# Optimization experiments

Hardware: AMD Instinct MI355X
Metric: run time of the kernel (lower is better)

The kernel has to match this reference:

```python
import jax, jax.numpy as jnp
import numpy as np


def setup_inputs() -> dict:
    key0 = jax.random.key(0)
    kq, kk, kv = jax.random.split(key0, 3)
    B, S, E = 4, 2048, 1024
    query = jax.random.normal(kq, (B, S, E), dtype=jnp.float32)
    key = jax.random.normal(kk, (B, S, E), dtype=jnp.float32)
    value = jax.random.normal(kv, (B, S, E), dtype=jnp.float32)
    attn_mask = jnp.zeros((B, S, S), dtype=jnp.float32)
    return {"query": query, "key": key, "value": value, "attn_mask": attn_mask}


def reference(query, key, value, attn_mask):
    # qk = Q K^T / sqrt(E) + mask; softmax over last dim; dropout is
    # identity in eval mode (reference baseline); out = attn @ V.
    E = query.shape[-1]
    scale = 1.0 / jnp.sqrt(jnp.asarray(E, dtype=query.dtype))
    qk = jnp.einsum("bqe,bke->bqk", query, key) * scale + attn_mask
    attn = jax.nn.softmax(qk, axis=-1)
    out = jnp.einsum("bqk,bke->bqe", attn, value)
    return out
```

## Files before the change

### kernel.cpp

```cpp
#include <hip/hip_runtime.h>
#include <stdint.h>
#include <math.h>

typedef unsigned short u16;
typedef short bf16x8 __attribute__((ext_vector_type(8)));
typedef unsigned short u16x8 __attribute__((ext_vector_type(8)));
typedef unsigned short u16x4 __attribute__((ext_vector_type(4)));
typedef float f32x4 __attribute__((ext_vector_type(4)));

#define LOG2E 1.4426950408889634f

__device__ __forceinline__ float bf2f(u16 u) {
  union { unsigned int i; float f; } v; v.i = ((unsigned int)u) << 16; return v.f;
}
__device__ __forceinline__ u16 f2bf(float f) {
  union { float ff; unsigned int i; } v; v.ff = f;
  unsigned int x = v.i;
  return (u16)((x + 0x7FFFu + ((x >> 16) & 1u)) >> 16);
}

__global__ __launch_bounds__(256)
void cvt_f32_bf16(const float* __restrict__ src, u16* __restrict__ dst, long n)
{
  long i = ((long)blockIdx.x * 256 + threadIdx.x) * 8;
  if (i + 8 > n) return;
  f32x4 a = *(const f32x4*)&src[i];
  f32x4 b = *(const f32x4*)&src[i + 4];
  u16x8 o;
#pragma unroll
  for (int j = 0; j < 4; j++) { o[j] = f2bf(a[j]); o[4 + j] = f2bf(b[j]); }
  *(u16x8*)&dst[i] = o;
}

__global__ __launch_bounds__(256)
void transcvt_v(const float* __restrict__ V, u16* __restrict__ VT, int S, int E)
{
  __shared__ u16 t[64][72];
  const int b = blockIdx.z;
  const float* Vb = V + (long)b * S * E;
  u16* VTb = VT + (long)b * S * E;
  const int k0 = blockIdx.x * 64, n0 = blockIdx.y * 64;
  const int tid = threadIdx.x;
#pragma unroll
  for (int p = 0; p < 2; p++) {
    int kk = p * 32 + (tid >> 3);
    int nn = (tid & 7) * 8;
    f32x4 a = *(const f32x4*)&Vb[(long)(k0 + kk) * E + n0 + nn];
    f32x4 c = *(const f32x4*)&Vb[(long)(k0 + kk) * E + n0 + nn + 4];
#pragma unroll
    for (int j = 0; j < 4; j++) { t[nn + j][kk] = f2bf(a[j]); t[nn + 4 + j][kk] = f2bf(c[j]); }
  }
  __syncthreads();
#pragma unroll
  for (int p = 0; p < 2; p++) {
    int nn = p * 32 + (tid >> 3);
    int kk = (tid & 7) * 8;
    u16x8 u;
#pragma unroll
    for (int j = 0; j < 8; j++) u[j] = t[nn][kk + j];
    *(u16x8*)&VTb[(long)(n0 + nn) * S + k0 + kk] = u;
  }
}

template<int ASRC, int BSRC, int BMODE, int HASMASK, int COUT>
__global__ __launch_bounds__(256, 2)
void gemm_bt(const void* __restrict__ Ap, int lda, long aRowOff,
             const void* __restrict__ Bp, int ldb, long bBatchStride,
             void* __restrict__ Cp, int ldc, long cRowOff,
             const float* __restrict__ maskf,
             int K, float scale, long g0, int S)
{
  const int tid  = threadIdx.x;
  const int lane = tid & 63;
  const int wave = tid >> 6;
  const long gTile = g0 + (long)blockIdx.y * 128;
  const int  b     = (int)(gTile / S);
  const int  nTile = blockIdx.x * 128;

  __shared__ u16 As[128][40];
  __shared__ u16 Bs[128][40];

  const int qm = (wave >> 1) * 64;
  const int qn = (wave & 1) * 64;

  f32x4 acc[4][4];
#pragma unroll
  for (int i = 0; i < 4; i++)
#pragma unroll
    for (int j = 0; j < 4; j++) acc[i][j] = (f32x4){0.f, 0.f, 0.f, 0.f};

  const u16*   Ab = (const u16*)Ap   + (gTile - aRowOff) * (long)lda;
  const float* Af = (const float*)Ap + (gTile - aRowOff) * (long)lda;
  const u16*   Bb = (const u16*)Bp   + (long)b * bBatchStride;
  const float* Bf = (const float*)Bp + (long)b * bBatchStride;

  const int lm = lane & 15;
  const int lk = (lane >> 4) * 8;

  for (int k0 = 0; k0 < K; k0 += 32) {
    if (ASRC == 0) {
      int srow = tid >> 2, scol = (tid & 3) * 8;
#pragma unroll
      for (int p = 0; p < 2; p++) {
        int r = p * 64 + srow;
        *(u16x8*)&As[r][scol] = *(const u16x8*)&Ab[(long)r * lda + k0 + scol];
      }
    } else {
      int srow = tid >> 3, scol = (tid & 7) * 4;
#pragma unroll
      for (int p = 0; p < 4; p++) {
        int r = p * 32 + srow;
        f32x4 a = *(const f32x4*)&Af[(long)r * lda + k0 + scol];
        u16x4 o;
#pragma unroll
        for (int j = 0; j < 4; j++) o[j] = f2bf(a[j]);
        *(u16x4*)&As[r][scol] = o;
      }
    }
    if (BMODE == 0) {
      if (BSRC == 0) {
        int srow = tid >> 2, scol = (tid & 3) * 8;
#pragma unroll
        for (int p = 0; p < 2; p++) {
          int r = p * 64 + srow;
          *(u16x8*)&Bs[r][scol] = *(const u16x8*)&Bb[(long)(nTile + r) * ldb + k0 + scol];
        }
      } else {
        int srow = tid >> 3, scol = (tid & 7) * 4;
#pragma unroll
        for (int p = 0; p < 4; p++) {
          int r = p * 32 + srow;
          f32x4 a = *(const f32x4*)&Bf[(long)(nTile + r) * ldb + k0 + scol];
          u16x4 o;
#pragma unroll
          for (int j = 0; j < 4; j++) o[j] = f2bf(a[j]);
          *(u16x4*)&Bs[r][scol] = o;
        }
      }
    }
    __syncthreads();

    bf16x8 af[4], bfr[4];
#pragma unroll
    for (int rt = 0; rt < 4; rt++)
      af[rt] = *(const bf16x8*)&As[qm + rt * 16 + lm][lk];
    if (BMODE == 0) {
#pragma unroll
      for (int ct = 0; ct < 4; ct++)
        bfr[ct] = *(const bf16x8*)&Bs[qn + ct * 16 + lm][lk];
    } else {
#pragma unroll
      for (int ct = 0; ct < 4; ct++) {
        const float* vp = Bf + (long)(k0 + lk) * ldb + nTile + qn + ct * 16 + lm;
#pragma unroll
        for (int j = 0; j < 8; j++) bfr[ct][j] = (short)f2bf(vp[(long)j * ldb]);
      }
    }
#pragma unroll
    for (int rt = 0; rt < 4; rt++)
#pragma unroll
      for (int ct = 0; ct < 4; ct++)
        acc[rt][ct] = __builtin_amdgcn_mfma_f32_16x16x32_bf16(af[rt], bfr[ct], acc[rt][ct], 0, 0, 0);
    __syncthreads();
  }

  const int lr = (lane >> 4) * 4;
#pragma unroll
  for (int rt = 0; rt < 4; rt++) {
#pragma unroll
    for (int ct = 0; ct < 4; ct++) {
      long gr = gTile + qm + rt * 16 + lr;
      int  cc = nTile + qn + ct * 16 + lm;
#pragma unroll
      for (int i = 0; i < 4; i++) {
        float v = acc[rt][ct][i] * scale;
        if (HASMASK) v += maskf[(gr + i) * (long)ldc + cc];
        if (COUT == 0)
          ((u16*)Cp)[(gr + i - cRowOff) * (long)ldc + cc] = f2bf(v);
        else
          ((float*)Cp)[(gr + i - cRowOff) * (long)ldc + cc] = v;
      }
    }
  }
}

__global__ __launch_bounds__(256)
void softmax_rows(u16* __restrict__ Sbuf, int ncols)
{
  const long row = blockIdx.x;
  u16* rp = Sbuf + row * (long)ncols;
  const int tid = threadIdx.x;

  u16x8 u = *(const u16x8*)&rp[tid * 8];
  float x[8];
  float m = -3.0e38f;
#pragma unroll
  for (int i = 0; i < 8; i++) { x[i] = bf2f(u[i]); m = fmaxf(m, x[i]); }
#pragma unroll
  for (int off = 32; off; off >>= 1) m = fmaxf(m, __shfl_xor(m, off, 64));
  __shared__ float redm[4];
  if ((tid & 63) == 0) redm[tid >> 6] = m;
  __syncthreads();
  m = fmaxf(fmaxf(redm[0], redm[1]), fmaxf(redm[2], redm[3]));

  float e[8];
  float s = 0.f;
#pragma unroll
  for (int i = 0; i < 8; i++) { e[i] = exp2f((x[i] - m) * LOG2E); s += e[i]; }
#pragma unroll
  for (int off = 32; off; off >>= 1) s += __shfl_xor(s, off, 64);
  __shared__ float reds[4];
  if ((tid & 63) == 0) reds[tid >> 6] = s;
  __syncthreads();
  s = reds[0] + reds[1] + reds[2] + reds[3];

  float inv = 1.0f / s;
  u16x8 o;
#pragma unroll
  for (int i = 0; i < 8; i++) o[i] = f2bf(e[i] * inv);
  *(u16x8*)&rp[tid * 8] = o;
}

extern "C" void kernel_launch(void* const* d_in, const int* in_sizes, int n_in,
                              void* d_out, int out_size, void* d_ws, size_t ws_size,
                              hipStream_t stream)
{
  const float* Q    = (const float*)d_in[0];
  const float* Km   = (const float*)d_in[1];
  const float* V    = (const float*)d_in[2];
  const float* mask = (const float*)d_in[3];
  float* out = (float*)d_out;

  const long qsz = in_sizes[0];
  const long msz = in_sizes[3];
  const long E = 1024;
  const long S = (msz / qsz) * E;
  const long B = qsz / (S * E);
  const long G = B * S;
  const float scale = 1.0f / sqrtf((float)E);

  const size_t convBytes = (size_t)(3 * qsz) * 2;
  const size_t rowBytes  = (size_t)S * 2;
  char* w = (char*)d_ws;
  size_t avail = ws_size;
  const bool haveConv = (ws_size >= convBytes + 128 * rowBytes);

  u16 *Qb = nullptr, *Kb = nullptr, *VTb = nullptr;
  if (haveConv) {
    Qb  = (u16*)w;              w += (size_t)qsz * 2;
    Kb  = (u16*)w;              w += (size_t)qsz * 2;
    VTb = (u16*)w;              w += (size_t)qsz * 2;
    avail -= convBytes;
  }
  long Rmax = (long)((avail / rowBytes) / 128) * 128;
  if (Rmax > G) Rmax = G;
  if (Rmax < 128) Rmax = 128;
  u16* Sbuf = (u16*)w;

  if (haveConv) {
    cvt_f32_bf16<<<dim3((unsigned)(qsz / 2048)), 256, 0, stream>>>(Q, Qb, qsz);
    cvt_f32_bf16<<<dim3((unsigned)(qsz / 2048)), 256, 0, stream>>>(Km, Kb, qsz);
    transcvt_v<<<dim3(S / 64, E / 64, B), 256, 0, stream>>>(V, VTb, (int)S, (int)E);
  }

  for (long g0 = 0; g0 < G; g0 += Rmax) {
    const long R = (G - g0 < Rmax) ? (G - g0) : Rmax;
    if (haveConv) {
      gemm_bt<0, 0, 0, 1, 0><<<dim3(S / 128, R / 128), 256, 0, stream>>>(
          Qb, (int)E, 0L, Kb, (int)E, S * E,
          Sbuf, (int)S, g0, mask, (int)E, scale, g0, (int)S);
    } else {
      gemm_bt<1, 1, 0, 1, 0><<<dim3(S / 128, R / 128), 256, 0, stream>>>(
          Q, (int)E, 0L, Km, (int)E, S * E,
          Sbuf, (int)S, g0, mask, (int)E, scale, g0, (int)S);
    }
    softmax_rows<<<dim3(R), 256, 0, stream>>>(Sbuf, (int)S);
    if (haveConv) {
      gemm_bt<0, 0, 0, 0, 1><<<dim3(E / 128, R / 128), 256, 0, stream>>>(
          Sbuf, (int)S, g0, VTb, (int)S, E * S,
          out, (int)E, 0L, nullptr, (int)S, 1.0f, g0, (int)S);
    } else {
      gemm_bt<0, 1, 1, 0, 1><<<dim3(E / 128, R / 128), 256, 0, stream>>>(
          Sbuf, (int)S, g0, V, (int)E, S * E,
          out, (int)E, 0L, nullptr, (int)S, 1.0f, g0, (int)S);
    }
  }
}
```

Measured before the change: 302.4 us.

## Double-buffer GEMM LDS tiles and fuse Q/K bf16 conversion into QK GEMM

```diff
diff --git a/kernel.cpp b/kernel.cpp
--- a/kernel.cpp
+++ b/kernel.cpp
@@ -5,7 +5,6 @@
 typedef unsigned short u16;
 typedef short bf16x8 __attribute__((ext_vector_type(8)));
 typedef unsigned short u16x8 __attribute__((ext_vector_type(8)));
-typedef unsigned short u16x4 __attribute__((ext_vector_type(4)));
 typedef float f32x4 __attribute__((ext_vector_type(4)));
 
 #define LOG2E 1.4426950408889634f
@@ -17,19 +16,6 @@
   union { float ff; unsigned int i; } v; v.ff = f;
   unsigned int x = v.i;
   return (u16)((x + 0x7FFFu + ((x >> 16) & 1u)) >> 16);
-}
-
-__global__ __launch_bounds__(256)
-void cvt_f32_bf16(const float* __restrict__ src, u16* __restrict__ dst, long n)
-{
-  long i = ((long)blockIdx.x * 256 + threadIdx.x) * 8;
-  if (i + 8 > n) return;
-  f32x4 a = *(const f32x4*)&src[i];
-  f32x4 b = *(const f32x4*)&src[i + 4];
-  u16x8 o;
-#pragma unroll
-  for (int j = 0; j < 4; j++) { o[j] = f2bf(a[j]); o[4 + j] = f2bf(b[j]); }
-  *(u16x8*)&dst[i] = o;
 }
 
 __global__ __launch_bounds__(256)
@@ -62,10 +48,10 @@
   }
 }
 
-template<int ASRC, int BSRC, int BMODE, int HASMASK, int COUT>
+template<int ASRC_F32, int BSRC_F32, int HASMASK, int COUT>
 __global__ __launch_bounds__(256, 2)
-void gemm_bt(const void* __restrict__ Ap, int lda, long aRowOff,
-             const void* __restrict__ Bp, int ldb, long bBatchStride,
+void gemm_pl(const void* __restrict__ A_, int lda, long aRowOff,
+             const void* __restrict__ B_, int ldb, long bBatchStride,
              void* __restrict__ Cp, int ldc, long cRowOff,
              const float* __restrict__ maskf,
              int K, float scale, long g0, int S)
@@ -77,100 +63,123 @@
   const int  b     = (int)(gTile / S);
   const int  nTile = blockIdx.x * 128;
 
-  __shared__ u16 As[128][40];
-  __shared__ u16 Bs[128][40];
+  __shared__ u16 lds[16384];
+
+  const float* Af = (const float*)A_ + (gTile - aRowOff) * (long)lda;
+  const u16*   Ab = (const u16*)A_   + (gTile - aRowOff) * (long)lda;
+  const float* Bf = (const float*)B_ + (long)b * bBatchStride;
+  const u16*   Bb = (const u16*)B_   + (long)b * bBatchStride;
+
+  const int row0 = wave * 16 + (lane & 15);
+  const int col8 = (lane >> 4) * 8;
+  const long aoff0 = (long)row0 * lda + col8;
+  const long aoff1 = aoff0 + (long)64 * lda;
+  const long boff0 = (long)(nTile + row0) * ldb + col8;
+  const long boff1 = boff0 + (long)64 * ldb;
+  const int idx0 = wave * 512 + lane * 8;
+  const int idx1 = idx0 + 2048;
+
+  f32x4 acc[4][4];
+#pragma unroll
+  for (int i = 0; i < 4; i++)
+#pragma unroll
+    for (int j = 0; j < 4; j++) acc[i][j] = (f32x4){0.f, 0.f, 0.f, 0.f};
+
+  const int qmi = (wave >> 1) * 4;
+  const int qni = (wave & 1) * 4;
+
+  f32x4 fa0a, fa0b, fa1a, fa1b, fb0a, fb0b, fb1a, fb1b;
+  u16x8 ua0, ua1, ub0, ub1;
+
+#define LOAD_STEP(k0)                                                        \
+  do {                                                                       \
+    if (ASRC_F32) {                                                          \
+      fa0a = *(const f32x4*)&Af[aoff0 + (k0)];                               \
+      fa0b = *(const f32x4*)&Af[aoff0 + (k0) + 4];                           \
+      fa1a = *(const f32x4*)&Af[aoff1 + (k0)];                               \
+      fa1b = *(const f32x4*)&Af[aoff1 + (k0) + 4];                           \
+    } else {                                                                 \
+      ua0 = *(const u16x8*)&Ab[aoff0 + (k0)];                                \
+      ua1 = *(const u16x8*)&Ab[aoff1 + (k0)];                                \
+    }                                                                        \
+    if (BSRC_F32) {                                                          \
+      fb0a = *(const f32x4*)&Bf[boff0 + (k0)];                               \
+      fb0b = *(const f32x4*)&Bf[boff0 + (k0) + 4];                           \
+      fb1a = *(const f32x4*)&Bf[boff1 + (k0)];                               \
+      fb1b = *(const f32x4*)&Bf[boff1 + (k0) + 4];                           \
+    } else {                                                                 \
+      ub0 = *(const u16x8*)&Bb[boff0 + (k0)];                                \
+      ub1 = *(const u16x8*)&Bb[boff1 + (k0)];                                \
+    }                                                                        \
+  } while (0)
+
+#define WRITE_STEP(bufOff)                                                   \
+  do {                                                                       \
+    if (ASRC_F32) {                                                          \
+      u16x8 w0, w1;                                                          \
+      _Pragma("unroll")                                                      \
+      for (int j = 0; j < 4; j++) {                                          \
+        w0[j] = f2bf(fa0a[j]); w0[4 + j] = f2bf(fa0b[j]);                    \
+        w1[j] = f2bf(fa1a[j]); w1[4 + j] = f2bf(fa1b[j]);                    \
+      }                                                                      \
+      *(u16x8*)&lds[(bufOff) + idx0] = w0;                                   \
+      *(u16x8*)&lds[(bufOff) + idx1] = w1;                                   \
+    } else {                                                                 \
+      *(u16x8*)&lds[(bufOff) + idx0] = ua0;                                  \
+      *(u16x8*)&lds[(bufOff) + idx1] = ua1;                                  \
+    }                                                                        \
+    if (BSRC_F32) {                                                          \
+      u16x8 w0, w1;                                                          \
+      _Pragma("unroll")                                                      \
+      for (int j = 0; j < 4; j++) {                                          \
+        w0[j] = f2bf(fb0a[j]); w0[4 + j] = f2bf(fb0b[j]);                    \
+        w1[j] = f2bf(fb1a[j]); w1[4 + j] = f2bf(fb1b[j]);                    \
+      }                                                                      \
+      *(u16x8*)&lds[(bufOff) + 4096 + idx0] = w0;                            \
+      *(u16x8*)&lds[(bufOff) + 4096 + idx1] = w1;                            \
+    } else {                                                                 \
+      *(u16x8*)&lds[(bufOff) + 4096 + idx0] = ub0;                           \
+      *(u16x8*)&lds[(bufOff) + 4096 + idx1] = ub1;                           \
+    }                                                                        \
+  } while (0)
+
+  const int Ksteps = K / 32;
+  LOAD_STEP(0);
+  WRITE_STEP(0);
+
+  int cb = 0;
+  for (int i = 0; i < Ksteps; ++i) {
+    __syncthreads();
+    const int cOff = cb * 8192;
+    if (i + 1 < Ksteps) LOAD_STEP((i + 1) * 32);
+    bf16x8 af[4], bfr[4];
+#pragma unroll
+    for (int rt = 0; rt < 4; rt++)
+      af[rt] = *(const bf16x8*)&lds[cOff + (qmi + rt) * 512 + lane * 8];
+#pragma unroll
+    for (int ct = 0; ct < 4; ct++)
+      bfr[ct] = *(const bf16x8*)&lds[cOff + 4096 + (qni + ct) * 512 + lane * 8];
+#pragma unroll
+    for (int rt = 0; rt < 4; rt++)
+#pragma unroll
+      for (int ct = 0; ct < 4; ct++)
+        acc[rt][ct] = __builtin_amdgcn_mfma_f32_16x16x32_bf16(af[rt], bfr[ct], acc[rt][ct], 0, 0, 0);
+    if (i + 1 < Ksteps) WRITE_STEP((cb ^ 1) * 8192);
+    cb ^= 1;
+  }
+#undef LOAD_STEP
+#undef WRITE_STEP
 
   const int qm = (wave >> 1) * 64;
   const int qn = (wave & 1) * 64;
-
-  f32x4 acc[4][4];
-#pragma unroll
-  for (int i = 0; i < 4; i++)
-#pragma unroll
-    for (int j = 0; j < 4; j++) acc[i][j] = (f32x4){0.f, 0.f, 0.f, 0.f};
-
-  const u16*   Ab = (const u16*)Ap   + (gTile - aRowOff) * (long)lda;
-  const float* Af = (const float*)Ap + (gTile - aRowOff) * (long)lda;
-  const u16*   Bb = (const u16*)Bp   + (long)b * bBatchStride;
-  const float* Bf = (const float*)Bp + (long)b * bBatchStride;
-
-  const int lm = lane & 15;
-  const int lk = (lane >> 4) * 8;
-
-  for (int k0 = 0; k0 < K; k0 += 32) {
-    if (ASRC == 0) {
-      int srow = tid >> 2, scol = (tid & 3) * 8;
-#pragma unroll
-      for (int p = 0; p < 2; p++) {
-        int r = p * 64 + srow;
-        *(u16x8*)&As[r][scol] = *(const u16x8*)&Ab[(long)r * lda + k0 + scol];
-      }
-    } else {
-      int srow = tid >> 3, scol = (tid & 7) * 4;
-#pragma unroll
-      for (int p = 0; p < 4; p++) {
-        int r = p * 32 + srow;
-        f32x4 a = *(const f32x4*)&Af[(long)r * lda + k0 + scol];
-        u16x4 o;
-#pragma unroll
-        for (int j = 0; j < 4; j++) o[j] = f2bf(a[j]);
-        *(u16x4*)&As[r][scol] = o;
-      }
-    }
-    if (BMODE == 0) {
-      if (BSRC == 0) {
-        int srow = tid >> 2, scol = (tid & 3) * 8;
-#pragma unroll
-        for (int p = 0; p < 2; p++) {
-          int r = p * 64 + srow;
-          *(u16x8*)&Bs[r][scol] = *(const u16x8*)&Bb[(long)(nTile + r) * ldb + k0 + scol];
-        }
-      } else {
-        int srow = tid >> 3, scol = (tid & 7) * 4;
-#pragma unroll
-        for (int p = 0; p < 4; p++) {
-          int r = p * 32 + srow;
-          f32x4 a = *(const f32x4*)&Bf[(long)(nTile + r) * ldb + k0 + scol];
-          u16x4 o;
-#pragma unroll
-          for (int j = 0; j < 4; j++) o[j] = f2bf(a[j]);
-          *(u16x4*)&Bs[r][scol] = o;
-        }
-      }
-    }
-    __syncthreads();
-
-    bf16x8 af[4], bfr[4];
-#pragma unroll
-    for (int rt = 0; rt < 4; rt++)
-      af[rt] = *(const bf16x8*)&As[qm + rt * 16 + lm][lk];
-    if (BMODE == 0) {
-#pragma unroll
-      for (int ct = 0; ct < 4; ct++)
-        bfr[ct] = *(const bf16x8*)&Bs[qn + ct * 16 + lm][lk];
-    } else {
-#pragma unroll
-      for (int ct = 0; ct < 4; ct++) {
-        const float* vp = Bf + (long)(k0 + lk) * ldb + nTile + qn + ct * 16 + lm;
-#pragma unroll
-        for (int j = 0; j < 8; j++) bfr[ct][j] = (short)f2bf(vp[(long)j * ldb]);
-      }
-    }
-#pragma unroll
-    for (int rt = 0; rt < 4; rt++)
-#pragma unroll
-      for (int ct = 0; ct < 4; ct++)
-        acc[rt][ct] = __builtin_amdgcn_mfma_f32_16x16x32_bf16(af[rt], bfr[ct], acc[rt][ct], 0, 0, 0);
-    __syncthreads();
-  }
-
+  const int lm16 = lane & 15;
   const int lr = (lane >> 4) * 4;
 #pragma unroll
   for (int rt = 0; rt < 4; rt++) {
 #pragma unroll
     for (int ct = 0; ct < 4; ct++) {
       long gr = gTile + qm + rt * 16 + lr;
-      int  cc = nTile + qn + ct * 16 + lm;
+      int  cc = nTile + qn + ct * 16 + lm16;
 #pragma unroll
       for (int i = 0; i < 4; i++) {
         float v = acc[rt][ct][i] * scale;
@@ -239,50 +248,26 @@
   const long G = B * S;
   const float scale = 1.0f / sqrtf((float)E);
 
-  const size_t convBytes = (size_t)(3 * qsz) * 2;
-  const size_t rowBytes  = (size_t)S * 2;
+  const size_t vtBytes  = (size_t)qsz * 2;
+  const size_t rowBytes = (size_t)S * 2;
   char* w = (char*)d_ws;
-  size_t avail = ws_size;
-  const bool haveConv = (ws_size >= convBytes + 128 * rowBytes);
-
-  u16 *Qb = nullptr, *Kb = nullptr, *VTb = nullptr;
-  if (haveConv) {
-    Qb  = (u16*)w;              w += (size_t)qsz * 2;
-    Kb  = (u16*)w;              w += (size_t)qsz * 2;
-    VTb = (u16*)w;              w += (size_t)qsz * 2;
-    avail -= convBytes;
-  }
+  u16* VTb = (u16*)w;  w += vtBytes;
+  size_t avail = (ws_size > vtBytes) ? ws_size - vtBytes : 0;
   long Rmax = (long)((avail / rowBytes) / 128) * 128;
   if (Rmax > G) Rmax = G;
   if (Rmax < 128) Rmax = 128;
   u16* Sbuf = (u16*)w;
 
-  if (haveConv) {
-    cvt_f32_bf16<<<dim3((unsigned)(qsz / 2048)), 256, 0, stream>>>(Q, Qb, qsz);
-    cvt_f32_bf16<<<dim3((unsigned)(qsz / 2048)), 256, 0, stream>>>(Km, Kb, qsz);
-    transcvt_v<<<dim3(S / 64, E / 64, B), 256, 0, stream>>>(V, VTb, (int)S, (int)E);
-  }
+  transcvt_v<<<dim3(S / 64, E / 64, B), 256, 0, stream>>>(V, VTb, (int)S, (int)E);
 
   for (long g0 = 0; g0 < G; g0 += Rmax) {
     const long R = (G - g0 < Rmax) ? (G - g0) : Rmax;
-    if (haveConv) {
-      gemm_bt<0, 0, 0, 1, 0><<<dim3(S / 128, R / 128), 256, 0, stream>>>(
-          Qb, (int)E, 0L, Kb, (int)E, S * E,
-          Sbuf, (int)S, g0, mask, (int)E, scale, g0, (int)S);
-    } else {
-      gemm_bt<1, 1, 0, 1, 0><<<dim3(S / 128, R / 128), 256, 0, stream>>>(
-          Q, (int)E, 0L, Km, (int)E, S * E,
-          Sbuf, (int)S, g0, mask, (int)E, scale, g0, (int)S);
-    }
+    gemm_pl<1, 1, 1, 0><<<dim3(S / 128, R / 128), 256, 0, stream>>>(
+        Q, (int)E, 0L, Km, (int)E, S * E,
+        Sbuf, (int)S, g0, mask, (int)E, scale, g0, (int)S);
     softmax_rows<<<dim3(R), 256, 0, stream>>>(Sbuf, (int)S);
-    if (haveConv) {
-      gemm_bt<0, 0, 0, 0, 1><<<dim3(E / 128, R / 128), 256, 0, stream>>>(
-          Sbuf, (int)S, g0, VTb, (int)S, E * S,
-          out, (int)E, 0L, nullptr, (int)S, 1.0f, g0, (int)S);
-    } else {
-      gemm_bt<0, 1, 1, 0, 1><<<dim3(E / 128, R / 128), 256, 0, stream>>>(
-          Sbuf, (int)S, g0, V, (int)E, S * E,
-          out, (int)E, 0L, nullptr, (int)S, 1.0f, g0, (int)S);
-    }
-  }
-}
+    gemm_pl<0, 0, 0, 1><<<dim3(E / 128, R / 128), 256, 0, stream>>>(
+        Sbuf, (int)S, g0, VTb, (int)S, E * S,
+        out, (int)E, 0L, nullptr, (int)S, 1.0f, g0, (int)S);
+  }
+}
```

Result: slower. 360.4 us (+19.2%).
